# Performance work log

Measured on AMD Instinct MI355X. Metric: run time of the kernel, lower is better.

## Reference

```python
import jax, jax.numpy as jnp
import numpy as np

B, L, H = 16, 2048, 768
V, D = 30000, 64


def setup_inputs() -> dict:
    key = jax.random.key(0)
    k1, k2, k3, k4 = jax.random.split(key, 4)
    bert_x = jax.random.normal(k1, (B, L, H), dtype=jnp.float32)
    x = jax.random.randint(k2, (B, L), 0, V, dtype=jnp.int64)
    ae = jax.random.normal(k3, (V, D), dtype=jnp.float32)
    w = jax.random.normal(k4, (D, D), dtype=jnp.float32)
    return {"bert_x": bert_x, "x": x, "ae": ae, "w": w}


def reference(bert_x, x, ae, w):
    # E[b,i] = ae[x[b,i]]  -> [B, L, D]
    E = ae[x]
    # fac[b,i,j] = E[b,i] @ w @ E[b,j]   (bilinear pairwise score)
    scores = jnp.einsum('bid,de,bje->bij', E, w, E)
    Lseq = bert_x.shape[1]
    i = jnp.arange(Lseq, dtype=bert_x.dtype)[:, None]
    j = jnp.arange(Lseq, dtype=bert_x.dtype)[None, :]
    # strictly-causal weight (i+1)/(j+1) for i < j, zero elsewhere
    coef = jnp.where(i < j, (i + 1.0) / (j + 1.0), 0.0).astype(bert_x.dtype)
    # res[:, j] = bert_x[:, j] + sum_{i<j} bert_x[:, i] * coef[i,j] * fac[b,i,j]
    res = bert_x + jnp.einsum('bij,bih->bjh', scores * coef, bert_x)
    return res
```

## Files before the change

### kernel.cpp

```cpp
#include <hip/hip_runtime.h>

#define Bb 16
#define Ll 2048
#define Hh 768
#define Dd 64
#define Cc 64
#define HC 64
#define NT (Hh / HC)
#define NCH (Ll / Cc)
#define PSEG 8
#define CPS (NCH / PSEG)
#define NHT (HC / 16)

typedef __attribute__((ext_vector_type(8))) short bf16x8;
typedef __attribute__((ext_vector_type(4))) float f32x4;

__device__ __forceinline__ short f2bf(float f) {
  union { float f; unsigned u; } c;
  c.f = f;
  unsigned r = (c.u + 0x7FFFu + ((c.u >> 16) & 1u)) >> 16;
  return (short)r;
}
__device__ __forceinline__ unsigned pack2(float a, float b) {
  return (unsigned)(unsigned short)f2bf(a) | ((unsigned)(unsigned short)f2bf(b) << 16);
}
__device__ __forceinline__ float bf2f(short s) {
  union { unsigned u; float f; } c;
  c.u = ((unsigned)(unsigned short)s) << 16;
  return c.f;
}

__device__ __forceinline__ void sync_lds() {
  asm volatile("s_waitcnt lgkmcnt(0)\n\ts_barrier" ::: "memory");
}

__global__ __launch_bounds__(256) void prep_kernel(const int* __restrict__ x,
                                                   const float* __restrict__ ae,
                                                   const float* __restrict__ w,
                                                   short* __restrict__ Eg,
                                                   short* __restrict__ FTg,
                                                   short* __restrict__ scTg) {
  const int tid = threadIdx.x;
  const int wv = tid >> 6, lane = tid & 63, quad = lane >> 4, lq = lane & 15;
  const int b = blockIdx.x >> 5, ch = blockIdx.x & 31;
  const size_t gb = (size_t)blockIdx.x * 4096;
  __shared__ short sE[64 * 64];
  __shared__ short sWT[64 * 64];
  __shared__ short sF[64 * 64];

  {
    const int i = tid >> 2, seg = tid & 3;
    const int idx = x[b * Ll + ch * Cc + i];
    const float4* aer = (const float4*)(ae + (size_t)idx * Dd) + seg * 4;
    float4 ev[4];
#pragma unroll
    for (int q = 0; q < 4; ++q) ev[q] = aer[q];
    uint4 pA, pB;
    pA.x = pack2(ev[0].x, ev[0].y); pA.y = pack2(ev[0].z, ev[0].w);
    pA.z = pack2(ev[1].x, ev[1].y); pA.w = pack2(ev[1].z, ev[1].w);
    pB.x = pack2(ev[2].x, ev[2].y); pB.y = pack2(ev[2].z, ev[2].w);
    pB.z = pack2(ev[3].x, ev[3].y); pB.w = pack2(ev[3].z, ev[3].w);
    *(uint4*)&sE[i * 64 + (((2 * seg) ^ (i & 7)) << 3)] = pA;
    *(uint4*)&sE[i * 64 + (((2 * seg + 1) ^ (i & 7)) << 3)] = pB;
    *(uint4*)(Eg + gb + i * 64 + seg * 16) = pA;
    *(uint4*)(Eg + gb + i * 64 + seg * 16 + 8) = pB;
    const float4* wr = (const float4*)w;
#pragma unroll
    for (int q = 0; q < 4; ++q) {
      const int fl = q * 256 + tid;
      const int d = fl >> 4, es = (fl & 15) * 4;
      const float4 v = wr[fl];
      const float vv[4] = {v.x, v.y, v.z, v.w};
#pragma unroll
      for (int c = 0; c < 4; ++c) {
        const int e = es + c;
        sWT[e * 64 + (((d >> 3) ^ (e & 7)) << 3) + (d & 7)] = f2bf(vv[c]);
      }
    }
  }
  __syncthreads();

  const int rm = wv * 16 + lq;
  bf16x8 aE[2], aW[2];
#pragma unroll
  for (int ks = 0; ks < 2; ++ks) {
    const int blk = ((ks * 4 + quad) ^ (rm & 7)) << 3;
    aE[ks] = *(const bf16x8*)&sE[rm * 64 + blk];
    aW[ks] = *(const bf16x8*)&sWT[rm * 64 + blk];
  }

#pragma unroll
  for (int nt = 0; nt < 4; ++nt) {
    const int rn = nt * 16 + lq;
    f32x4 accF = {}, accT = {};
#pragma unroll
    for (int ks = 0; ks < 2; ++ks) {
      const int blk = ((ks * 4 + quad) ^ (rn & 7)) << 3;
      const bf16x8 bW = *(const bf16x8*)&sWT[rn * 64 + blk];
      const bf16x8 bE = *(const bf16x8*)&sE[rn * 64 + blk];
      accF = __builtin_amdgcn_mfma_f32_16x16x32_bf16(aE[ks], bW, accF, 0, 0, 0);
      accT = __builtin_amdgcn_mfma_f32_16x16x32_bf16(aW[ks], bE, accT, 0, 0, 0);
    }
#pragma unroll
    for (int r = 0; r < 4; ++r) {
      const int i = wv * 16 + quad * 4 + r;
      const int e = nt * 16 + lq;
      sF[i * 64 + (((e >> 3) ^ (i & 7)) << 3) + (e & 7)] = f2bf(accF[r]);
      const int e2 = wv * 16 + quad * 4 + r;
      const int i2 = nt * 16 + lq;
      FTg[gb + e2 * 64 + i2] = f2bf(accT[r]);
    }
  }
  __syncthreads();

#pragma unroll
  for (int nt = 0; nt < 4; ++nt) {
    const int rn = nt * 16 + lq;
    f32x4 acc = {};
#pragma unroll
    for (int ks = 0; ks < 2; ++ks) {
      const int blk = ((ks * 4 + quad) ^ (rn & 7)) << 3;
      const bf16x8 bF = *(const bf16x8*)&sF[rn * 64 + blk];
      acc = __builtin_amdgcn_mfma_f32_16x16x32_bf16(aE[ks], bF, acc, 0, 0, 0);
    }
#pragma unroll
    for (int r = 0; r < 4; ++r) {
      const int j = wv * 16 + quad * 4 + r;
      const int i = nt * 16 + lq;
      scTg[gb + j * 64 + i] = f2bf(i < j ? acc[r] : 0.f);
    }
  }
}

__global__ __launch_bounds__(256) void state_kernel(const float* __restrict__ bx,
                                                    const short* __restrict__ FTg,
                                                    short* __restrict__ Sg) {
  const int tile = blockIdx.x, b = blockIdx.y, seg = blockIdx.z;
  const int tid = threadIdx.x;
  const int w = tid >> 6, lane = tid & 63, quad = lane >> 4, lq = lane & 15;
  const int ip = tid & 31, hg = tid >> 5;
  const int rj = w * 16 + lq;

  __shared__ short sGT[2][HC * 64];

  f32x4 accS[NHT] = {};
  float2 rG[2 * NHT];
  bf16x8 bD[2];

  auto load_G = [&](int ch) {
    const float* xr = bx + ((size_t)(b * Ll) + ch * Cc + 2 * ip) * Hh + tile * HC + hg * 8;
#pragma unroll
    for (int k = 0; k < NHT; ++k) {
      rG[k] = *(const float2*)(xr + 2 * k);
      rG[NHT + k] = *(const float2*)(xr + Hh + 2 * k);
    }
  };
  auto load_D = [&](int ch) {
    const size_t tb = (size_t)(b * NCH + ch) * 4096;
#pragma unroll
    for (int ks = 0; ks < 2; ++ks)
      bD[ks] = *(const bf16x8*)(FTg + tb + rj * 64 + (ks * 4 + quad) * 8);
  };

  load_G(seg * CPS);
  load_D(seg * CPS);

#pragma unroll
  for (int c = 0; c < CPS; ++c) {
    const int ch = seg * CPS + c;
    const int cur = c & 1;
    const int p0 = ch * Cc;
    {
      const float s0 = (float)(p0 + 2 * ip + 1), s1 = (float)(p0 + 2 * ip + 2);
#pragma unroll
      for (int k = 0; k < NHT; ++k)
#pragma unroll
        for (int cc = 0; cc < 2; ++cc) {
          const int h = hg * 8 + 2 * k + cc;
          const float g0 = (cc ? rG[k].y : rG[k].x) * s0;
          const float g1 = (cc ? rG[NHT + k].y : rG[NHT + k].x) * s1;
          const int sa = h * 64 + (((ip >> 2) ^ (h & 7)) << 3) + 2 * (ip & 3);
          *(unsigned*)&sGT[cur][sa] = pack2(g0, g1);
        }
    }
    if (c + 1 < CPS) load_G(ch + 1);
    sync_lds();
#pragma unroll
    for (int ht = 0; ht < NHT; ++ht) {
      const int rh = ht * 16 + lq;
#pragma unroll
      for (int ks = 0; ks < 2; ++ks) {
        const int blk = ((ks * 4 + quad) ^ (rh & 7)) << 3;
        const bf16x8 g = *(const bf16x8*)&sGT[cur][rh * 64 + blk];
        accS[ht] = __builtin_amdgcn_mfma_f32_16x16x32_bf16(g, bD[ks], accS[ht], 0, 0, 0);
      }
    }
    if (c + 1 < CPS) load_D(ch + 1);
  }

  short* Sr = Sg + (size_t)(b * (PSEG - 1) + seg) * (Hh * 64);
#pragma unroll
  for (int ht = 0; ht < NHT; ++ht)
#pragma unroll
    for (int r = 0; r < 4; ++r) {
      const int h = tile * HC + ht * 16 + quad * 4 + r;
      Sr[h * 64 + w * 16 + lq] = f2bf(accS[ht][r]);
    }
}

__global__ __launch_bounds__(256) void scan_kernel(const float* __restrict__ bx,
                                                   const short* __restrict__ Eg,
                                                   const short* __restrict__ FTg,
                                                   const short* __restrict__ scTg,
                                                   const short* __restrict__ Sg,
                                                   float* __restrict__ out) {
  const int tile = blockIdx.x, b = blockIdx.y, seg = blockIdx.z;
  const int tid = threadIdx.x;
  const int w = tid >> 6, lane = tid & 63, quad = lane >> 4, lq = lane & 15;
  const int ip = tid & 31, hg = tid >> 5;
  const int rj = w * 16 + lq;

  __shared__ short sGT[2][HC * 64];
  __shared__ short sST[2][HC * 64];

  f32x4 accS[NHT] = {};
  bf16x8 aC1[2], aC2[2], bD[2];
  float2 rG[2 * NHT];

  auto load_G = [&](int ch) {
    const float* xr = bx + ((size_t)(b * Ll) + ch * Cc + 2 * ip) * Hh + tile * HC + hg * 8;
#pragma unroll
    for (int k = 0; k < NHT; ++k) {
      rG[k] = *(const float2*)(xr + 2 * k);
      rG[NHT + k] = *(const float2*)(xr + Hh + 2 * k);
    }
  };
  auto load_frag = [&](int ch) {
    const size_t tb = (size_t)(b * NCH + ch) * 4096;
#pragma unroll
    for (int ks = 0; ks < 2; ++ks) {
      const int o = rj * 64 + (ks * 4 + quad) * 8;
      aC1[ks] = *(const bf16x8*)(scTg + tb + o);
      aC2[ks] = *(const bf16x8*)(Eg + tb + o);
      bD[ks]  = *(const bf16x8*)(FTg + tb + o);
    }
  };

  load_G(seg * CPS);
  load_frag(seg * CPS);

  for (int s = 0; s < seg; ++s) {
    const short* Sr = Sg + (size_t)(b * (PSEG - 1) + s) * (Hh * 64);
#pragma unroll
    for (int ht = 0; ht < NHT; ++ht)
#pragma unroll
      for (int r = 0; r < 4; ++r) {
        const int h = tile * HC + ht * 16 + quad * 4 + r;
        accS[ht][r] += bf2f(Sr[h * 64 + w * 16 + lq]);
      }
  }

#pragma unroll
  for (int c = 0; c < CPS; ++c) {
    const int ch = seg * CPS + c;
    const int cur = c & 1;
    const int p0 = ch * Cc;
    {
      const float s0 = (float)(p0 + 2 * ip + 1), s1 = (float)(p0 + 2 * ip + 2);
#pragma unroll
      for (int k = 0; k < NHT; ++k)
#pragma unroll
        for (int cc = 0; cc < 2; ++cc) {
          const int h = hg * 8 + 2 * k + cc;
          const float g0 = (cc ? rG[k].y : rG[k].x) * s0;
          const float g1 = (cc ? rG[NHT + k].y : rG[NHT + k].x) * s1;
          const int sa = h * 64 + (((ip >> 2) ^ (h & 7)) << 3) + 2 * (ip & 3);
          *(unsigned*)&sGT[cur][sa] = pack2(g0, g1);
        }
    }
#pragma unroll
    for (int ht = 0; ht < NHT; ++ht)
#pragma unroll
      for (int r = 0; r < 4; ++r) {
        const int h = ht * 16 + quad * 4 + r;
        const int d = w * 16 + lq;
        sST[cur][h * 64 + (((d >> 3) ^ (h & 7)) << 3) + (d & 7)] = f2bf(accS[ht][r]);
      }
    if (c + 1 < CPS) load_G(ch + 1);
    sync_lds();

    f32x4 accO[NHT] = {};
#pragma unroll
    for (int ht = 0; ht < NHT; ++ht) {
      const int rh = ht * 16 + lq;
#pragma unroll
      for (int ks = 0; ks < 2; ++ks) {
        const int blk = ((ks * 4 + quad) ^ (rh & 7)) << 3;
        const bf16x8 g  = *(const bf16x8*)&sGT[cur][rh * 64 + blk];
        const bf16x8 st = *(const bf16x8*)&sST[cur][rh * 64 + blk];
        accO[ht] = __builtin_amdgcn_mfma_f32_16x16x32_bf16(aC1[ks], g,  accO[ht], 0, 0, 0);
        accO[ht] = __builtin_amdgcn_mfma_f32_16x16x32_bf16(aC2[ks], st, accO[ht], 0, 0, 0);
        accS[ht] = __builtin_amdgcn_mfma_f32_16x16x32_bf16(g, bD[ks],  accS[ht], 0, 0, 0);
      }
    }
    if (c + 1 < CPS) load_frag(ch + 1);

#pragma unroll
    for (int ht = 0; ht < NHT; ++ht)
#pragma unroll
      for (int r = 0; r < 4; ++r) {
        const int gj = p0 + w * 16 + quad * 4 + r;
        const size_t off = ((size_t)(b * Ll) + gj) * Hh + tile * HC + ht * 16 + lq;
        out[off] = bx[off] + accO[ht][r] * (1.0f / (float)(gj + 1));
      }
  }
}

extern "C" void kernel_launch(void* const* d_in, const int* in_sizes, int n_in,
                              void* d_out, int out_size, void* d_ws, size_t ws_size,
                              hipStream_t stream) {
  (void)in_sizes; (void)n_in; (void)out_size; (void)ws_size;
  const float* bx = (const float*)d_in[0];
  const int* x = (const int*)d_in[1];
  const float* ae = (const float*)d_in[2];
  const float* w = (const float*)d_in[3];
  float* out = (float*)d_out;
  short* Eg = (short*)d_ws;
  short* FTg = Eg + (size_t)512 * 4096;
  short* scTg = FTg + (size_t)512 * 4096;
  short* Sg = scTg + (size_t)512 * 4096;

  prep_kernel<<<Bb * NCH, 256, 0, stream>>>(x, ae, w, Eg, FTg, scTg);
  dim3 gst(NT, Bb, PSEG - 1);
  state_kernel<<<gst, 256, 0, stream>>>(bx, FTg, Sg);
  dim3 gsc(NT, Bb, PSEG);
  scan_kernel<<<gsc, 256, 0, stream>>>(bx, Eg, FTg, scTg, Sg, out);
}
```

Baseline: 254.0 us.

## Double sequence segments, add fp32 prefix kernel over segment states, remap block IDs

The number of sequence segments goes from 8 to 16, so the scan and state kernels launch more blocks and each block runs a shorter serial chain. Per-segment states are now stored in fp32, and a new prefix_kernel sums them across segments so each scan block reads one precomputed prefix instead of looping over all earlier segments. Block indices are flattened and remapped to group 8 segments per tile, and the bert_x loads are widened to float4. This adds a launch and more fp32 state traffic (about 2x workspace for Sg) in exchange for more parallelism and less redundant prefix work per block.

Result: slower. 295.3 us (+16.2%).

```diff
diff --git a/kernel.cpp b/kernel.cpp
--- a/kernel.cpp
+++ b/kernel.cpp
@@ -8,7 +8,7 @@
 #define HC 64
 #define NT (Hh / HC)
 #define NCH (Ll / Cc)
-#define PSEG 8
+#define PSEG 16
 #define CPS (NCH / PSEG)
 #define NHT (HC / 16)
 
@@ -23,11 +23,6 @@
 }
 __device__ __forceinline__ unsigned pack2(float a, float b) {
   return (unsigned)(unsigned short)f2bf(a) | ((unsigned)(unsigned short)f2bf(b) << 16);
-}
-__device__ __forceinline__ float bf2f(short s) {
-  union { unsigned u; float f; } c;
-  c.u = ((unsigned)(unsigned short)s) << 16;
-  return c.f;
 }
 
 __device__ __forceinline__ void sync_lds() {
@@ -134,8 +129,12 @@
 
 __global__ __launch_bounds__(256) void state_kernel(const float* __restrict__ bx,
                                                     const short* __restrict__ FTg,
-                                                    short* __restrict__ Sg) {
-  const int tile = blockIdx.x, b = blockIdx.y, seg = blockIdx.z;
+                                                    float* __restrict__ Sg) {
+  const int id = blockIdx.x;
+  const int t12 = id >> 3;
+  const int tile = t12 % NT;
+  const int g = ((t12 / NT) << 3) | (id & 7);
+  const int b = g / (PSEG - 1), seg = g % (PSEG - 1);
   const int tid = threadIdx.x;
   const int w = tid >> 6, lane = tid & 63, quad = lane >> 4, lq = lane & 15;
   const int ip = tid & 31, hg = tid >> 5;
@@ -144,16 +143,15 @@
   __shared__ short sGT[2][HC * 64];
 
   f32x4 accS[NHT] = {};
-  float2 rG[2 * NHT];
+  float4 rGa[2], rGb[2];
   bf16x8 bD[2];
 
   auto load_G = [&](int ch) {
     const float* xr = bx + ((size_t)(b * Ll) + ch * Cc + 2 * ip) * Hh + tile * HC + hg * 8;
-#pragma unroll
-    for (int k = 0; k < NHT; ++k) {
-      rG[k] = *(const float2*)(xr + 2 * k);
-      rG[NHT + k] = *(const float2*)(xr + Hh + 2 * k);
-    }
+    rGa[0] = *(const float4*)(xr);
+    rGa[1] = *(const float4*)(xr + 4);
+    rGb[0] = *(const float4*)(xr + Hh);
+    rGb[1] = *(const float4*)(xr + Hh + 4);
   };
   auto load_D = [&](int ch) {
     const size_t tb = (size_t)(b * NCH + ch) * 4096;
@@ -172,16 +170,16 @@
     const int p0 = ch * Cc;
     {
       const float s0 = (float)(p0 + 2 * ip + 1), s1 = (float)(p0 + 2 * ip + 2);
-#pragma unroll
-      for (int k = 0; k < NHT; ++k)
-#pragma unroll
-        for (int cc = 0; cc < 2; ++cc) {
-          const int h = hg * 8 + 2 * k + cc;
-          const float g0 = (cc ? rG[k].y : rG[k].x) * s0;
-          const float g1 = (cc ? rG[NHT + k].y : rG[NHT + k].x) * s1;
-          const int sa = h * 64 + (((ip >> 2) ^ (h & 7)) << 3) + 2 * (ip & 3);
-          *(unsigned*)&sGT[cur][sa] = pack2(g0, g1);
-        }
+      const float A[8] = {rGa[0].x, rGa[0].y, rGa[0].z, rGa[0].w,
+                          rGa[1].x, rGa[1].y, rGa[1].z, rGa[1].w};
+      const float Bv[8] = {rGb[0].x, rGb[0].y, rGb[0].z, rGb[0].w,
+                           rGb[1].x, rGb[1].y, rGb[1].z, rGb[1].w};
+#pragma unroll
+      for (int e = 0; e < 8; ++e) {
+        const int h = hg * 8 + e;
+        const int sa = h * 64 + (((ip >> 2) ^ (h & 7)) << 3) + 2 * (ip & 3);
+        *(unsigned*)&sGT[cur][sa] = pack2(A[e] * s0, Bv[e] * s1);
+      }
     }
     if (c + 1 < CPS) load_G(ch + 1);
     sync_lds();
@@ -191,30 +189,50 @@
 #pragma unroll
       for (int ks = 0; ks < 2; ++ks) {
         const int blk = ((ks * 4 + quad) ^ (rh & 7)) << 3;
-        const bf16x8 g = *(const bf16x8*)&sGT[cur][rh * 64 + blk];
-        accS[ht] = __builtin_amdgcn_mfma_f32_16x16x32_bf16(g, bD[ks], accS[ht], 0, 0, 0);
+        const bf16x8 gv = *(const bf16x8*)&sGT[cur][rh * 64 + blk];
+        accS[ht] = __builtin_amdgcn_mfma_f32_16x16x32_bf16(gv, bD[ks], accS[ht], 0, 0, 0);
       }
     }
     if (c + 1 < CPS) load_D(ch + 1);
   }
 
-  short* Sr = Sg + (size_t)(b * (PSEG - 1) + seg) * (Hh * 64);
+  float* Sr = Sg + (size_t)(b * (PSEG - 1) + seg) * (Hh * Dd);
 #pragma unroll
   for (int ht = 0; ht < NHT; ++ht)
 #pragma unroll
     for (int r = 0; r < 4; ++r) {
       const int h = tile * HC + ht * 16 + quad * 4 + r;
-      Sr[h * 64 + w * 16 + lq] = f2bf(accS[ht][r]);
-    }
+      Sr[h * 64 + w * 16 + lq] = accS[ht][r];
+    }
+}
+
+__global__ __launch_bounds__(256) void prefix_kernel(float* __restrict__ Sg) {
+  const int b = blockIdx.x / 48;
+  const int v = (blockIdx.x % 48) * 256 + threadIdx.x;
+  float4* base = (float4*)(Sg + (size_t)b * (PSEG - 1) * (Hh * Dd)) + v;
+  const int stride = Hh * Dd / 4;
+  float4 va[PSEG - 1];
+#pragma unroll
+  for (int s = 0; s < PSEG - 1; ++s) va[s] = base[s * stride];
+  float4 acc = va[0];
+#pragma unroll
+  for (int s = 1; s < PSEG - 1; ++s) {
+    acc.x += va[s].x; acc.y += va[s].y; acc.z += va[s].z; acc.w += va[s].w;
+    base[s * stride] = acc;
+  }
 }
 
 __global__ __launch_bounds__(256) void scan_kernel(const float* __restrict__ bx,
                                                    const short* __restrict__ Eg,
                                                    const short* __restrict__ FTg,
                                                    const short* __restrict__ scTg,
-                                                   const short* __restrict__ Sg,
+                                                   const float* __restrict__ Sg,
                                                    float* __restrict__ out) {
-  const int tile = blockIdx.x, b = blockIdx.y, seg = blockIdx.z;
+  const int id = blockIdx.x;
+  const int t12 = id >> 3;
+  const int tile = t12 % NT;
+  const int g = ((t12 / NT) << 3) | (id & 7);
+  const int b = g >> 4, seg = g & 15;
   const int tid = threadIdx.x;
   const int w = tid >> 6, lane = tid & 63, quad = lane >> 4, lq = lane & 15;
   const int ip = tid & 31, hg = tid >> 5;
@@ -225,15 +243,14 @@
 
   f32x4 accS[NHT] = {};
   bf16x8 aC1[2], aC2[2], bD[2];
-  float2 rG[2 * NHT];
+  float4 rGa[2], rGb[2];
 
   auto load_G = [&](int ch) {
     const float* xr = bx + ((size_t)(b * Ll) + ch * Cc + 2 * ip) * Hh + tile * HC + hg * 8;
-#pragma unroll
-    for (int k = 0; k < NHT; ++k) {
-      rG[k] = *(const float2*)(xr + 2 * k);
-      rG[NHT + k] = *(const float2*)(xr + Hh + 2 * k);
-    }
+    rGa[0] = *(const float4*)(xr);
+    rGa[1] = *(const float4*)(xr + 4);
+    rGb[0] = *(const float4*)(xr + Hh);
+    rGb[1] = *(const float4*)(xr + Hh + 4);
   };
   auto load_frag = [&](int ch) {
     const size_t tb = (size_t)(b * NCH + ch) * 4096;
@@ -249,14 +266,14 @@
   load_G(seg * CPS);
   load_frag(seg * CPS);
 
-  for (int s = 0; s < seg; ++s) {
-    const short* Sr = Sg + (size_t)(b * (PSEG - 1) + s) * (Hh * 64);
+  if (seg > 0) {
+    const float* Pr = Sg + (size_t)(b * (PSEG - 1) + (seg - 1)) * (Hh * Dd);
 #pragma unroll
     for (int ht = 0; ht < NHT; ++ht)
 #pragma unroll
       for (int r = 0; r < 4; ++r) {
         const int h = tile * HC + ht * 16 + quad * 4 + r;
-        accS[ht][r] += bf2f(Sr[h * 64 + w * 16 + lq]);
+        accS[ht][r] = Pr[h * 64 + w * 16 + lq];
       }
   }
 
@@ -267,16 +284,16 @@
     const int p0 = ch * Cc;
     {
       const float s0 = (float)(p0 + 2 * ip + 1), s1 = (float)(p0 + 2 * ip + 2);
-#pragma unroll
-      for (int k = 0; k < NHT; ++k)
-#pragma unroll
-        for (int cc = 0; cc < 2; ++cc) {
-          const int h = hg * 8 + 2 * k + cc;
-          const float g0 = (cc ? rG[k].y : rG[k].x) * s0;
-          const float g1 = (cc ? rG[NHT + k].y : rG[NHT + k].x) * s1;
-          const int sa = h * 64 + (((ip >> 2) ^ (h & 7)) << 3) + 2 * (ip & 3);
-          *(unsigned*)&sGT[cur][sa] = pack2(g0, g1);
-        }
+      const float A[8] = {rGa[0].x, rGa[0].y, rGa[0].z, rGa[0].w,
+                          rGa[1].x, rGa[1].y, rGa[1].z, rGa[1].w};
+      const float Bv[8] = {rGb[0].x, rGb[0].y, rGb[0].z, rGb[0].w,
+                           rGb[1].x, rGb[1].y, rGb[1].z, rGb[1].w};
+#pragma unroll
+      for (int e = 0; e < 8; ++e) {
+        const int h = hg * 8 + e;
+        const int sa = h * 64 + (((ip >> 2) ^ (h & 7)) << 3) + 2 * (ip & 3);
+        *(unsigned*)&sGT[cur][sa] = pack2(A[e] * s0, Bv[e] * s1);
+      }
     }
 #pragma unroll
     for (int ht = 0; ht < NHT; ++ht)
@@ -296,11 +313,11 @@
 #pragma unroll
       for (int ks = 0; ks < 2; ++ks) {
         const int blk = ((ks * 4 + quad) ^ (rh & 7)) << 3;
-        const bf16x8 g  = *(const bf16x8*)&sGT[cur][rh * 64 + blk];
+        const bf16x8 gv = *(const bf16x8*)&sGT[cur][rh * 64 + blk];
         const bf16x8 st = *(const bf16x8*)&sST[cur][rh * 64 + blk];
-        accO[ht] = __builtin_amdgcn_mfma_f32_16x16x32_bf16(aC1[ks], g,  accO[ht], 0, 0, 0);
+        accO[ht] = __builtin_amdgcn_mfma_f32_16x16x32_bf16(aC1[ks], gv, accO[ht], 0, 0, 0);
         accO[ht] = __builtin_amdgcn_mfma_f32_16x16x32_bf16(aC2[ks], st, accO[ht], 0, 0, 0);
-        accS[ht] = __builtin_amdgcn_mfma_f32_16x16x32_bf16(g, bD[ks],  accS[ht], 0, 0, 0);
+        accS[ht] = __builtin_amdgcn_mfma_f32_16x16x32_bf16(gv, bD[ks], accS[ht], 0, 0, 0);
       }
     }
     if (c + 1 < CPS) load_frag(ch + 1);
@@ -328,11 +345,10 @@
   short* Eg = (short*)d_ws;
   short* FTg = Eg + (size_t)512 * 4096;
   short* scTg = FTg + (size_t)512 * 4096;
-  short* Sg = scTg + (size_t)512 * 4096;
+  float* Sg = (float*)(scTg + (size_t)512 * 4096);
 
   prep_kernel<<<Bb * NCH, 256, 0, stream>>>(x, ae, w, Eg, FTg, scTg);
-  dim3 gst(NT, Bb, PSEG - 1);
-  state_kernel<<<gst, 256, 0, stream>>>(bx, FTg, Sg);
-  dim3 gsc(NT, Bb, PSEG);
-  scan_kernel<<<gsc, 256, 0, stream>>>(bx, Eg, FTg, scTg, Sg, out);
-}
+  state_kernel<<<NT * Bb * (PSEG - 1), 256, 0, stream>>>(bx, FTg, Sg);
+  prefix_kernel<<<Bb * 48, 256, 0, stream>>>(Sg);
+  scan_kernel<<<NT * Bb * PSEG, 256, 0, stream>>>(bx, Eg, FTg, scTg, Sg, out);
+}
```
